# Optimization experiments

Hardware: AMD Instinct MI355X
Metric: run time of the kernel (lower is better)

The kernel has to match this reference:

```python
import jax, jax.numpy as jnp
import numpy as np

N_NODES = 50000
N_EDGES = 600000
D = 128
REL_DIM = 100
N_REL = 40
NEG_SLOPE = 0.2


def setup_inputs() -> dict:
    key = jax.random.key(0)
    ks = jax.random.split(key, 9)
    return {
        "node_features": jax.random.normal(ks[0], (N_NODES, D), jnp.float32),
        "edge_index": jax.random.randint(ks[1], (2, N_EDGES), 0, N_NODES, jnp.int64 if jax.config.jax_enable_x64 else jnp.int32),
        "edge_type": jax.random.randint(ks[2], (N_EDGES,), 0, N_REL, jnp.int32),
        "W": jax.random.normal(ks[3], (D, D), jnp.float32) * (1.0 / np.sqrt(D)),
        "W_r": jax.random.normal(ks[4], (REL_DIM, D), jnp.float32) * (1.0 / np.sqrt(REL_DIM)),
        "a": jax.random.normal(ks[5], (3 * D,), jnp.float32) * (1.0 / np.sqrt(3 * D)),
        "W_res": jax.random.normal(ks[6], (D, D), jnp.float32) * (1.0 / np.sqrt(D)),
        "b_res": jax.random.normal(ks[7], (D,), jnp.float32) * 0.01,
        "rel_emb": jax.random.normal(ks[8], (N_REL, REL_DIM), jnp.float32),
    }


def _segment_softmax(logits, seg_ids, num_segments):
    # numerically stable softmax over edges grouped by destination node
    seg_max = jax.ops.segment_max(logits, seg_ids, num_segments=num_segments)
    seg_max = jnp.where(jnp.isfinite(seg_max), seg_max, 0.0)
    e = jnp.exp(logits - seg_max[seg_ids])
    seg_sum = jax.ops.segment_sum(e, seg_ids, num_segments=num_segments)
    return e / (seg_sum[seg_ids] + 1e-16)


def reference(node_features, edge_index, edge_type, W, W_r, a, W_res, b_res, rel_emb):
    src = edge_index[0]  # x_j (source / message sender)
    dst = edge_index[1]  # x_i (target / aggregation index)

    h = node_features @ W                      # [N, D]
    h_rel = rel_emb[edge_type] @ W_r           # [E, D]
    h_src = h[src]                             # [E, D]
    h_dst = h[dst]                             # [E, D]

    # attention logit per edge: a . cat(W x_i, W x_j, W_r r_e), LeakyReLU(0.2)
    logit = h_dst @ a[:D] + h_src @ a[D:2 * D] + h_rel @ a[2 * D:]  # [E]
    logit = jax.nn.leaky_relu(logit, NEG_SLOPE)

    alpha = _segment_softmax(logit, dst, N_NODES)  # [E]

    agg = jax.ops.segment_sum(h_src * alpha[:, None], dst, num_segments=N_NODES)  # [N, D]

    out = agg + node_features @ W_res + b_res  # residual connection
    # LayerG: SELU then dropout (identity in eval mode)
    return jax.nn.selu(out)
```

## Files before the change

kernel.cpp:

```cpp
#include <hip/hip_runtime.h>
#include <hip/hip_bf16.h>

typedef __attribute__((ext_vector_type(8))) short bf16x8;
typedef __attribute__((ext_vector_type(4))) float f32x4;

#define LDS_STRIDE 528
#define CAP 64
#define TROWS 32
#define CHUNK 4096
#define BSHIFT 6
#define NBUCK_MAX 832
#define BUCKCAP 1280

__device__ __forceinline__ unsigned short f2bf(float f) {
    union { float f; unsigned int u; } v; v.f = f;
    unsigned int r = (v.u + 0x7FFF + ((v.u >> 16) & 1)) >> 16;
    return (unsigned short)r;
}
__device__ __forceinline__ float bf2f(unsigned int hbits) {
    union { unsigned int u; float f; } v; v.u = hbits << 16;
    return v.f;
}

__global__ __launch_bounds__(256) void setup_kernel(
    const float* __restrict__ W, const float* __restrict__ W_res,
    unsigned short* __restrict__ WbPack,
    const float* __restrict__ W_r, const float* __restrict__ a,
    const float* __restrict__ rel_emb, float* __restrict__ rl,
    int n_rel, int rel_dim,
    unsigned int* __restrict__ cursor, int NBUCK)
{
    __shared__ float a3[128];
    __shared__ float wa[128];
    int bid = blockIdx.x;
    int tid = threadIdx.x;

    if (bid < 16) {
        int g = bid * 256 + tid;
        int t = g >> 8;
        int s = (g >> 6) & 3;
        int lane = g & 63;
        int ncol = ((t & 7) << 4) + (lane & 15);
        int k0 = s * 32 + ((lane >> 4) << 3);
        const float* srcw = (t < 8) ? W : W_res;
        unsigned short* dstp = WbPack + ((size_t)(t * 4 + s) * 64 + lane) * 8;
        #pragma unroll
        for (int j = 0; j < 8; ++j) dstp[j] = f2bf(srcw[(size_t)(k0 + j) * 128 + ncol]);
        return;
    }
    if (bid == 16) {
        if (tid < 128) a3[tid] = a[256 + tid];
        __syncthreads();
        if (tid < rel_dim) {
            float s = 0.f;
            for (int d = 0; d < 128; ++d) s += W_r[tid * 128 + d] * a3[d];
            wa[tid] = s;
        }
        __syncthreads();
        if (tid < n_rel) {
            float s = 0.f;
            for (int k = 0; k < rel_dim; ++k) s += rel_emb[tid * rel_dim + k] * wa[k];
            rl[tid] = s;
        }
        return;
    }
    for (int i = tid; i < NBUCK; i += 256) cursor[i] = 0u;
}

__global__ __launch_bounds__(256) void gemm_scatter_kernel(
    const float* __restrict__ X, const unsigned short* __restrict__ WbPack,
    const float* __restrict__ b_res, const float* __restrict__ a,
    unsigned short* __restrict__ hb, unsigned short* __restrict__ resb,
    float* __restrict__ p, float* __restrict__ q, int M,
    const int* __restrict__ src, const int* __restrict__ dst_i, const int* __restrict__ etype,
    unsigned int* __restrict__ cursor, unsigned int* __restrict__ binned,
    int E, int NC, int NBUCK)
{
    __shared__ __align__(16) unsigned char smem[TROWS * LDS_STRIDE];
    __shared__ float pq_s[128];
    const int tid = threadIdx.x;
    const int bid = blockIdx.x;

    const bool isC = (bid < 2 * NC) && (bid & 1);
    if (isC) {
        const int k = bid >> 1;
        unsigned int* hist = (unsigned int*)smem;
        unsigned int* offs = hist + NBUCK_MAX;
        for (int i = tid; i < NBUCK; i += 256) hist[i] = 0;
        __syncthreads();
        unsigned int dcache[CHUNK / 256];
        unsigned int pk1[CHUNK / 256];
        #pragma unroll
        for (int i = 0; i < CHUNK / 256; ++i) {
            int e = k * CHUNK + i * 256 + tid;
            dcache[i] = 0xffffffffu;
            if (e < E) {
                unsigned int d = (unsigned int)__builtin_nontemporal_load(dst_i + e);
                unsigned int s = (unsigned int)__builtin_nontemporal_load(src + e);
                unsigned int t = (unsigned int)__builtin_nontemporal_load(etype + e);
                pk1[i] = (s << 16) | ((t & 63u) << 10);
                unsigned int r = atomicAdd(&hist[d >> BSHIFT], 1u);
                dcache[i] = (r << 20) | d;
            }
        }
        __syncthreads();
        for (int i = tid; i < NBUCK; i += 256) {
            unsigned int h = hist[i];
            offs[i] = h ? atomicAdd(&cursor[i], h) : 0u;
        }
        __syncthreads();
        #pragma unroll
        for (int i = 0; i < CHUNK / 256; ++i) {
            unsigned int dc = dcache[i];
            if (dc != 0xffffffffu) {
                unsigned int d = dc & 0xfffffu;
                unsigned int bk = d >> BSHIFT;
                unsigned int r = (dc >> 20) + offs[bk];
                if (r < BUCKCAP)
                    binned[(size_t)bk * BUCKCAP + r] = pk1[i] | (d & 63u);
            }
        }
        return;
    }
    const int gid = (bid < 2 * NC) ? (bid >> 1) : (bid - NC);

    const int lane = tid & 63;
    const int wave = tid >> 6;
    const int rowbase = gid * TROWS;
    const int c16 = lane & 15;
    const int kq = lane >> 4;

    if (tid < 128) pq_s[tid] = 0.f;

    bf16x8 wfrag[4][4];
    #pragma unroll
    for (int tt = 0; tt < 4; ++tt)
        #pragma unroll
        for (int s = 0; s < 4; ++s)
            wfrag[tt][s] = *(const bf16x8*)(WbPack + ((size_t)((wave * 4 + tt) * 4 + s) * 64 + lane) * 8);

    float bres[4];
    #pragma unroll
    for (int tt = 0; tt < 4; ++tt) {
        int t = wave * 4 + tt;
        bres[tt] = (t >= 8) ? b_res[(t - 8) * 16 + c16] : 0.f;
    }
    float pa[4], qa[4];
    #pragma unroll
    for (int tt = 0; tt < 4; ++tt) {
        int col = (wave * 4 + tt) * 16 + c16;
        pa[tt] = (wave < 2) ? a[col] : 0.f;
        qa[tt] = (wave < 2) ? a[128 + col] : 0.f;
    }

    #pragma unroll
    for (int j = 0; j < (TROWS * 32) / 256; ++j) {
        int ch = j * 256 + tid;
        int r = ch >> 5;
        int c = ch & 31;
        int gr = rowbase + r; if (gr >= M) gr = M - 1;
        float4 v = *(const float4*)(X + (size_t)gr * 128 + c * 4);
        unsigned int u0 = ((unsigned)f2bf(v.y) << 16) | f2bf(v.x);
        unsigned int u1 = ((unsigned)f2bf(v.w) << 16) | f2bf(v.z);
        *(uint2*)(smem + r * LDS_STRIDE + c * 8) = make_uint2(u0, u1);
    }
    __syncthreads();

    f32x4 acc[2][4];
    #pragma unroll
    for (int rt = 0; rt < 2; ++rt)
        #pragma unroll
        for (int tt = 0; tt < 4; ++tt) acc[rt][tt] = (f32x4){0.f, 0.f, 0.f, 0.f};

    #pragma unroll
    for (int s = 0; s < 4; ++s) {
        #pragma unroll
        for (int rt = 0; rt < 2; ++rt) {
            int row = rt * 16 + c16;
            bf16x8 af = *(const bf16x8*)(smem + row * LDS_STRIDE + s * 64 + kq * 16);
            #pragma unroll
            for (int tt = 0; tt < 4; ++tt)
                acc[rt][tt] = __builtin_amdgcn_mfma_f32_16x16x32_bf16(af, wfrag[tt][s], acc[rt][tt], 0, 0, 0);
        }
    }
    __syncthreads();

    if (wave < 2) {
        #pragma unroll
        for (int rt = 0; rt < 2; ++rt) {
            #pragma unroll
            for (int i = 0; i < 4; ++i) {
                float pp = 0.f, qq = 0.f;
                #pragma unroll
                for (int tt = 0; tt < 4; ++tt) {
                    pp += acc[rt][tt][i] * pa[tt];
                    qq += acc[rt][tt][i] * qa[tt];
                }
                #pragma unroll
                for (int d = 1; d < 16; d <<= 1) {
                    pp += __shfl_xor(pp, d, 64);
                    qq += __shfl_xor(qq, d, 64);
                }
                if (c16 == 0) {
                    int r = rt * 16 + kq * 4 + i;
                    atomicAdd(&pq_s[r], pp);
                    atomicAdd(&pq_s[64 + r], qq);
                }
            }
        }
    }

    #pragma unroll
    for (int rt = 0; rt < 2; ++rt) {
        #pragma unroll
        for (int tt = 0; tt < 4; ++tt) {
            int colall = (wave * 4 + tt) * 16 + c16;
            #pragma unroll
            for (int i = 0; i < 4; ++i) {
                int row = rt * 16 + kq * 4 + i;
                *(unsigned short*)(smem + row * LDS_STRIDE + colall * 2) = f2bf(acc[rt][tt][i] + bres[tt]);
            }
        }
    }
    __syncthreads();

    #pragma unroll
    for (int j = 0; j < (TROWS * 16) / 256; ++j) {
        int ch = j * 256 + tid;
        int r = ch >> 4;
        int c = ch & 15;
        int gr = rowbase + r;
        uint4 hv = *(const uint4*)(smem + r * LDS_STRIDE + c * 16);
        uint4 rv = *(const uint4*)(smem + r * LDS_STRIDE + 256 + c * 16);
        if (gr < M) {
            *(uint4*)(hb + (size_t)gr * 128 + c * 8) = hv;
            *(uint4*)(resb + (size_t)gr * 128 + c * 8) = rv;
        }
    }
    if (tid < TROWS) {
        int gr = rowbase + tid;
        if (gr < M) { p[gr] = pq_s[tid]; q[gr] = pq_s[64 + tid]; }
    }
}

__global__ __launch_bounds__(512) void agg_kernel(
    const unsigned short* __restrict__ hb, const unsigned short* __restrict__ resb,
    const float* __restrict__ p, const float* __restrict__ q, const float* __restrict__ rl,
    const unsigned int* __restrict__ binned, const unsigned int* __restrict__ cursor,
    float* __restrict__ out, int N, int n_rel)
{
    __shared__ unsigned int slots_l[64 * CAP];
    __shared__ unsigned int cnt_l[64];
    __shared__ float rls[64];
    const int tid = threadIdx.x;
    const int b = blockIdx.x;

    if (tid < n_rel) rls[tid] = rl[tid];
    if (tid < 64) cnt_l[tid] = 0;
    __syncthreads();

    const size_t off = (size_t)b * BUCKCAP;
    const unsigned int tot = min(cursor[b], (unsigned int)BUCKCAP);
    for (unsigned int i = tid; i < tot; i += 512) {
        unsigned int pk = binned[off + i];
        unsigned int dl = pk & 63u;
        unsigned int r = atomicAdd(&cnt_l[dl], 1u);
        if (r < CAP) slots_l[dl * CAP + r] = pk;
    }
    __syncthreads();

    const int lane = tid & 63;
    const int wave = tid >> 6;
    const int sub = lane & 31;
    const int shbase = lane & 32;
    const unsigned short* hsub = hb + sub * 4;

    for (int round = 0; round < 4; ++round) {
        int dl = round * 16 + wave * 2 + (lane >> 5);
        int node = b * 64 + dl;
        if (node >= N) continue;
        int nn = min((int)cnt_l[dl], CAP);

        float pnode = p[node];
        uint2 rv = *(const uint2*)(resb + (size_t)node * 128 + sub * 4);
        float a0 = 0.f, a1 = 0.f, a2 = 0.f, a3 = 0.f;
        float ssum = 0.f;

        for (int c = 0; c < nn; c += 32) {
            int m = min(32, nn - c);
            float se = 0.f;
            int sv = 0;
            if (sub < m) {
                unsigned int pk = slots_l[dl * CAP + c + sub];
                sv = (int)(pk >> 16);
                int t = (int)((pk >> 10) & 63u);
                float l = pnode + q[sv] + rls[t];
                l = (l > 0.f) ? l : 0.2f * l;
                se = __expf(l);
            }
            ssum += se;

            int j = 0;
            for (; j + 7 < m; j += 8) {
                float w[8]; int r[8]; uint2 v[8];
                #pragma unroll
                for (int u = 0; u < 8; ++u) { w[u] = __shfl(se, shbase + j + u); r[u] = __shfl(sv, shbase + j + u); }
                #pragma unroll
                for (int u = 0; u < 8; ++u) v[u] = *(const uint2*)(hsub + (size_t)r[u] * 128);
                #pragma unroll
                for (int u = 0; u < 8; ++u) {
                    a0 += w[u] * bf2f(v[u].x & 0xffff);
                    a1 += w[u] * bf2f(v[u].x >> 16);
                    a2 += w[u] * bf2f(v[u].y & 0xffff);
                    a3 += w[u] * bf2f(v[u].y >> 16);
                }
            }
            for (; j + 3 < m; j += 4) {
                float w[4]; int r[4]; uint2 v[4];
                #pragma unroll
                for (int u = 0; u < 4; ++u) { w[u] = __shfl(se, shbase + j + u); r[u] = __shfl(sv, shbase + j + u); }
                #pragma unroll
                for (int u = 0; u < 4; ++u) v[u] = *(const uint2*)(hsub + (size_t)r[u] * 128);
                #pragma unroll
                for (int u = 0; u < 4; ++u) {
                    a0 += w[u] * bf2f(v[u].x & 0xffff);
                    a1 += w[u] * bf2f(v[u].x >> 16);
                    a2 += w[u] * bf2f(v[u].y & 0xffff);
                    a3 += w[u] * bf2f(v[u].y >> 16);
                }
            }
            for (; j < m; ++j) {
                float w = __shfl(se, shbase + j);
                int r = __shfl(sv, shbase + j);
                uint2 v = *(const uint2*)(hsub + (size_t)r * 128);
                a0 += w * bf2f(v.x & 0xffff);
                a1 += w * bf2f(v.x >> 16);
                a2 += w * bf2f(v.y & 0xffff);
                a3 += w * bf2f(v.y >> 16);
            }
        }

        #pragma unroll
        for (int d = 1; d < 32; d <<= 1) ssum += __shfl_xor(ssum, d, 64);
        float inv = 1.0f / (ssum + 1e-16f);
        a0 *= inv; a1 *= inv; a2 *= inv; a3 *= inv;

        float o0 = a0 + bf2f(rv.x & 0xffff), o1 = a1 + bf2f(rv.x >> 16);
        float o2 = a2 + bf2f(rv.y & 0xffff), o3 = a3 + bf2f(rv.y >> 16);
        const float SC = 1.0507009873554805f, AL = 1.6732632423543772f;
        o0 = (o0 > 0.f) ? SC * o0 : SC * AL * (__expf(o0) - 1.f);
        o1 = (o1 > 0.f) ? SC * o1 : SC * AL * (__expf(o1) - 1.f);
        o2 = (o2 > 0.f) ? SC * o2 : SC * AL * (__expf(o2) - 1.f);
        o3 = (o3 > 0.f) ? SC * o3 : SC * AL * (__expf(o3) - 1.f);
        f32x4 ov = (f32x4){o0, o1, o2, o3};
        __builtin_nontemporal_store(ov, (f32x4*)(out + (size_t)node * 128 + sub * 4));
    }
}

extern "C" void kernel_launch(void* const* d_in, const int* in_sizes, int n_in,
                              void* d_out, int out_size, void* d_ws, size_t ws_size,
                              hipStream_t stream)
{
    const float* X      = (const float*)d_in[0];
    const int*   ei     = (const int*)d_in[1];
    const int*   etype  = (const int*)d_in[2];
    const float* W      = (const float*)d_in[3];
    const float* W_r    = (const float*)d_in[4];
    const float* a      = (const float*)d_in[5];
    const float* W_res  = (const float*)d_in[6];
    const float* b_res  = (const float*)d_in[7];
    const float* rel_emb= (const float*)d_in[8];

    const int N = in_sizes[0] / 128;
    const int E = in_sizes[2];
    const int n_rel = in_sizes[8] / 100;
    const int* src = ei;
    const int* dst = ei + E;

    char* w = (char*)d_ws;
    auto alloc = [&](size_t bytes) -> void* {
        void* ptr = (void*)w;
        w += (bytes + 255) & ~(size_t)255;
        return ptr;
    };
    const int NC    = (E + CHUNK - 1) / CHUNK;
    const int NBUCK = (N + 63) >> BSHIFT;

    unsigned short* WbPack = (unsigned short*)alloc((size_t)16 * 4 * 64 * 8 * 2);
    unsigned short* hb     = (unsigned short*)alloc((size_t)N * 128 * 2);
    unsigned short* resb   = (unsigned short*)alloc((size_t)N * 128 * 2);
    float* p       = (float*)alloc((size_t)N * 4);
    float* q       = (float*)alloc((size_t)N * 4);
    float* rl      = (float*)alloc(64 * 4);
    unsigned int* cursor = (unsigned int*)alloc((size_t)NBUCK * 4);
    unsigned int* binned = (unsigned int*)alloc((size_t)NBUCK * BUCKCAP * 4);
    float* out     = (float*)d_out;

    const int gemm_blocks = (N + TROWS - 1) / TROWS;
    const int agg_blocks  = NBUCK;

    setup_kernel<<<18, 256, 0, stream>>>(W, W_res, WbPack, W_r, a, rel_emb, rl,
                                         n_rel, 100, cursor, NBUCK);
    gemm_scatter_kernel<<<gemm_blocks + NC, 256, 0, stream>>>(
        X, WbPack, b_res, a, hb, resb, p, q, N,
        src, dst, etype, cursor, binned, E, NC, NBUCK);
    agg_kernel<<<agg_blocks, 512, 0, stream>>>(hb, resb, p, q, rl, binned, cursor,
                                               out, N, n_rel);
}
```

Baseline: 147.5 us.

## Replace global bucket cursors with per-chunk fixed cells in edge binning

```diff
diff --git a/kernel.cpp b/kernel.cpp
--- a/kernel.cpp
+++ b/kernel.cpp
@@ -10,7 +10,7 @@
 #define CHUNK 4096
 #define BSHIFT 6
 #define NBUCK_MAX 832
-#define BUCKCAP 1280
+#define CELLCAP 32
 
 __device__ __forceinline__ unsigned short f2bf(float f) {
     union { float f; unsigned int u; } v; v.f = f;
@@ -27,8 +27,7 @@
     unsigned short* __restrict__ WbPack,
     const float* __restrict__ W_r, const float* __restrict__ a,
     const float* __restrict__ rel_emb, float* __restrict__ rl,
-    int n_rel, int rel_dim,
-    unsigned int* __restrict__ cursor, int NBUCK)
+    int n_rel, int rel_dim)
 {
     __shared__ float a3[128];
     __shared__ float wa[128];
@@ -48,23 +47,19 @@
         for (int j = 0; j < 8; ++j) dstp[j] = f2bf(srcw[(size_t)(k0 + j) * 128 + ncol]);
         return;
     }
-    if (bid == 16) {
-        if (tid < 128) a3[tid] = a[256 + tid];
-        __syncthreads();
-        if (tid < rel_dim) {
-            float s = 0.f;
-            for (int d = 0; d < 128; ++d) s += W_r[tid * 128 + d] * a3[d];
-            wa[tid] = s;
-        }
-        __syncthreads();
-        if (tid < n_rel) {
-            float s = 0.f;
-            for (int k = 0; k < rel_dim; ++k) s += rel_emb[tid * rel_dim + k] * wa[k];
-            rl[tid] = s;
-        }
-        return;
-    }
-    for (int i = tid; i < NBUCK; i += 256) cursor[i] = 0u;
+    if (tid < 128) a3[tid] = a[256 + tid];
+    __syncthreads();
+    if (tid < rel_dim) {
+        float s = 0.f;
+        for (int d = 0; d < 128; ++d) s += W_r[tid * 128 + d] * a3[d];
+        wa[tid] = s;
+    }
+    __syncthreads();
+    if (tid < n_rel) {
+        float s = 0.f;
+        for (int k = 0; k < rel_dim; ++k) s += rel_emb[tid * rel_dim + k] * wa[k];
+        rl[tid] = s;
+    }
 }
 
 __global__ __launch_bounds__(256) void gemm_scatter_kernel(
@@ -73,7 +68,7 @@
     unsigned short* __restrict__ hb, unsigned short* __restrict__ resb,
     float* __restrict__ p, float* __restrict__ q, int M,
     const int* __restrict__ src, const int* __restrict__ dst_i, const int* __restrict__ etype,
-    unsigned int* __restrict__ cursor, unsigned int* __restrict__ binned,
+    unsigned char* __restrict__ cnt, unsigned int* __restrict__ binned,
     int E, int NC, int NBUCK)
 {
     __shared__ __align__(16) unsigned char smem[TROWS * LDS_STRIDE];
@@ -85,7 +80,6 @@
     if (isC) {
         const int k = bid >> 1;
         unsigned int* hist = (unsigned int*)smem;
-        unsigned int* offs = hist + NBUCK_MAX;
         for (int i = tid; i < NBUCK; i += 256) hist[i] = 0;
         __syncthreads();
         unsigned int dcache[CHUNK / 256];
@@ -104,20 +98,17 @@
             }
         }
         __syncthreads();
-        for (int i = tid; i < NBUCK; i += 256) {
-            unsigned int h = hist[i];
-            offs[i] = h ? atomicAdd(&cursor[i], h) : 0u;
-        }
-        __syncthreads();
+        for (int i = tid; i < NBUCK; i += 256)
+            cnt[(size_t)i * NC + k] = (unsigned char)min(hist[i], 255u);
         #pragma unroll
         for (int i = 0; i < CHUNK / 256; ++i) {
             unsigned int dc = dcache[i];
             if (dc != 0xffffffffu) {
                 unsigned int d = dc & 0xfffffu;
                 unsigned int bk = d >> BSHIFT;
-                unsigned int r = (dc >> 20) + offs[bk];
-                if (r < BUCKCAP)
-                    binned[(size_t)bk * BUCKCAP + r] = pk1[i] | (d & 63u);
+                unsigned int r = dc >> 20;
+                if (r < CELLCAP)
+                    binned[((size_t)bk * NC + k) * CELLCAP + r] = pk1[i] | (d & 63u);
             }
         }
         return;
@@ -246,26 +237,30 @@
 __global__ __launch_bounds__(512) void agg_kernel(
     const unsigned short* __restrict__ hb, const unsigned short* __restrict__ resb,
     const float* __restrict__ p, const float* __restrict__ q, const float* __restrict__ rl,
-    const unsigned int* __restrict__ binned, const unsigned int* __restrict__ cursor,
-    float* __restrict__ out, int N, int n_rel)
+    const unsigned int* __restrict__ binned, const unsigned char* __restrict__ cnt,
+    float* __restrict__ out, int N, int n_rel, int NC)
 {
     __shared__ unsigned int slots_l[64 * CAP];
     __shared__ unsigned int cnt_l[64];
+    __shared__ unsigned char cntl[160];
     __shared__ float rls[64];
     const int tid = threadIdx.x;
     const int b = blockIdx.x;
 
     if (tid < n_rel) rls[tid] = rl[tid];
     if (tid < 64) cnt_l[tid] = 0;
-    __syncthreads();
-
-    const size_t off = (size_t)b * BUCKCAP;
-    const unsigned int tot = min(cursor[b], (unsigned int)BUCKCAP);
-    for (unsigned int i = tid; i < tot; i += 512) {
-        unsigned int pk = binned[off + i];
-        unsigned int dl = pk & 63u;
-        unsigned int r = atomicAdd(&cnt_l[dl], 1u);
-        if (r < CAP) slots_l[dl * CAP + r] = pk;
+    if (tid < NC) cntl[tid] = cnt[(size_t)b * NC + tid];
+    __syncthreads();
+
+    if (tid < NC) {
+        int n = min((int)cntl[tid], CELLCAP);
+        const unsigned int* cell = binned + ((size_t)b * NC + tid) * CELLCAP;
+        for (int j = 0; j < n; ++j) {
+            unsigned int pk = cell[j];
+            unsigned int dl = pk & 63u;
+            unsigned int r = atomicAdd(&cnt_l[dl], 1u);
+            if (r < CAP) slots_l[dl * CAP + r] = pk;
+        }
     }
     __syncthreads();
 
@@ -392,18 +387,18 @@
     float* p       = (float*)alloc((size_t)N * 4);
     float* q       = (float*)alloc((size_t)N * 4);
     float* rl      = (float*)alloc(64 * 4);
-    unsigned int* cursor = (unsigned int*)alloc((size_t)NBUCK * 4);
-    unsigned int* binned = (unsigned int*)alloc((size_t)NBUCK * BUCKCAP * 4);
+    unsigned char* cnt   = (unsigned char*)alloc((size_t)NBUCK * NC);
+    unsigned int* binned = (unsigned int*)alloc((size_t)NBUCK * NC * CELLCAP * 4);
     float* out     = (float*)d_out;
 
     const int gemm_blocks = (N + TROWS - 1) / TROWS;
     const int agg_blocks  = NBUCK;
 
-    setup_kernel<<<18, 256, 0, stream>>>(W, W_res, WbPack, W_r, a, rel_emb, rl,
-                                         n_rel, 100, cursor, NBUCK);
+    setup_kernel<<<17, 256, 0, stream>>>(W, W_res, WbPack, W_r, a, rel_emb, rl,
+                                         n_rel, 100);
     gemm_scatter_kernel<<<gemm_blocks + NC, 256, 0, stream>>>(
         X, WbPack, b_res, a, hb, resb, p, q, N,
-        src, dst, etype, cursor, binned, E, NC, NBUCK);
-    agg_kernel<<<agg_blocks, 512, 0, stream>>>(hb, resb, p, q, rl, binned, cursor,
-                                               out, N, n_rel);
-}
+        src, dst, etype, cnt, binned, E, NC, NBUCK);
+    agg_kernel<<<agg_blocks, 512, 0, stream>>>(hb, resb, p, q, rl, binned, cnt,
+                                               out, N, n_rel, NC);
+}
```

Measured after the change: 153.7 us. +4.3%, slower.

## Fuse setup, GEMM/scatter and aggregation into one cooperative persistent kernel

Applied to the files above, without the earlier changes.

```diff
diff --git a/kernel.cpp b/kernel.cpp
--- a/kernel.cpp
+++ b/kernel.cpp
@@ -1,5 +1,8 @@
 #include <hip/hip_runtime.h>
 #include <hip/hip_bf16.h>
+#include <hip/hip_cooperative_groups.h>
+
+namespace cg = cooperative_groups;
 
 typedef __attribute__((ext_vector_type(8))) short bf16x8;
 typedef __attribute__((ext_vector_type(4))) float f32x4;
@@ -22,338 +25,332 @@
     return v.f;
 }
 
-__global__ __launch_bounds__(256) void setup_kernel(
+__global__ __launch_bounds__(256) void fused_all(
+    const float* __restrict__ X,
     const float* __restrict__ W, const float* __restrict__ W_res,
+    const float* __restrict__ W_r, const float* __restrict__ av,
+    const float* __restrict__ b_res, const float* __restrict__ rel_emb,
+    const int* __restrict__ srcI, const int* __restrict__ dstI, const int* __restrict__ etypeI,
     unsigned short* __restrict__ WbPack,
-    const float* __restrict__ W_r, const float* __restrict__ a,
-    const float* __restrict__ rel_emb, float* __restrict__ rl,
-    int n_rel, int rel_dim,
-    unsigned int* __restrict__ cursor, int NBUCK)
+    unsigned short* __restrict__ hb, unsigned short* __restrict__ resb,
+    float* __restrict__ p, float* __restrict__ q, float* __restrict__ rl,
+    unsigned int* __restrict__ cursor, unsigned int* __restrict__ binned,
+    float* __restrict__ out,
+    int Nn, int E, int n_rel, int rel_dim, int NC, int NBUCK, int GT)
 {
-    __shared__ float a3[128];
-    __shared__ float wa[128];
-    int bid = blockIdx.x;
-    int tid = threadIdx.x;
-
-    if (bid < 16) {
-        int g = bid * 256 + tid;
-        int t = g >> 8;
-        int s = (g >> 6) & 3;
-        int lane = g & 63;
-        int ncol = ((t & 7) << 4) + (lane & 15);
-        int k0 = s * 32 + ((lane >> 4) << 3);
-        const float* srcw = (t < 8) ? W : W_res;
-        unsigned short* dstp = WbPack + ((size_t)(t * 4 + s) * 64 + lane) * 8;
-        #pragma unroll
-        for (int j = 0; j < 8; ++j) dstp[j] = f2bf(srcw[(size_t)(k0 + j) * 128 + ncol]);
-        return;
-    }
-    if (bid == 16) {
-        if (tid < 128) a3[tid] = a[256 + tid];
-        __syncthreads();
-        if (tid < rel_dim) {
-            float s = 0.f;
-            for (int d = 0; d < 128; ++d) s += W_r[tid * 128 + d] * a3[d];
-            wa[tid] = s;
-        }
-        __syncthreads();
-        if (tid < n_rel) {
-            float s = 0.f;
-            for (int k = 0; k < rel_dim; ++k) s += rel_emb[tid * rel_dim + k] * wa[k];
-            rl[tid] = s;
-        }
-        return;
-    }
-    for (int i = tid; i < NBUCK; i += 256) cursor[i] = 0u;
-}
-
-__global__ __launch_bounds__(256) void gemm_scatter_kernel(
-    const float* __restrict__ X, const unsigned short* __restrict__ WbPack,
-    const float* __restrict__ b_res, const float* __restrict__ a,
-    unsigned short* __restrict__ hb, unsigned short* __restrict__ resb,
-    float* __restrict__ p, float* __restrict__ q, int M,
-    const int* __restrict__ src, const int* __restrict__ dst_i, const int* __restrict__ etype,
-    unsigned int* __restrict__ cursor, unsigned int* __restrict__ binned,
-    int E, int NC, int NBUCK)
-{
+    cg::grid_group grid = cg::this_grid();
     __shared__ __align__(16) unsigned char smem[TROWS * LDS_STRIDE];
     __shared__ float pq_s[128];
-    const int tid = threadIdx.x;
-    const int bid = blockIdx.x;
-
-    const bool isC = (bid < 2 * NC) && (bid & 1);
-    if (isC) {
-        const int k = bid >> 1;
-        unsigned int* hist = (unsigned int*)smem;
-        unsigned int* offs = hist + NBUCK_MAX;
-        for (int i = tid; i < NBUCK; i += 256) hist[i] = 0;
-        __syncthreads();
-        unsigned int dcache[CHUNK / 256];
-        unsigned int pk1[CHUNK / 256];
-        #pragma unroll
-        for (int i = 0; i < CHUNK / 256; ++i) {
-            int e = k * CHUNK + i * 256 + tid;
-            dcache[i] = 0xffffffffu;
-            if (e < E) {
-                unsigned int d = (unsigned int)__builtin_nontemporal_load(dst_i + e);
-                unsigned int s = (unsigned int)__builtin_nontemporal_load(src + e);
-                unsigned int t = (unsigned int)__builtin_nontemporal_load(etype + e);
-                pk1[i] = (s << 16) | ((t & 63u) << 10);
-                unsigned int r = atomicAdd(&hist[d >> BSHIFT], 1u);
-                dcache[i] = (r << 20) | d;
-            }
-        }
-        __syncthreads();
-        for (int i = tid; i < NBUCK; i += 256) {
-            unsigned int h = hist[i];
-            offs[i] = h ? atomicAdd(&cursor[i], h) : 0u;
-        }
-        __syncthreads();
-        #pragma unroll
-        for (int i = 0; i < CHUNK / 256; ++i) {
-            unsigned int dc = dcache[i];
-            if (dc != 0xffffffffu) {
-                unsigned int d = dc & 0xfffffu;
-                unsigned int bk = d >> BSHIFT;
-                unsigned int r = (dc >> 20) + offs[bk];
-                if (r < BUCKCAP)
-                    binned[(size_t)bk * BUCKCAP + r] = pk1[i] | (d & 63u);
-            }
-        }
-        return;
-    }
-    const int gid = (bid < 2 * NC) ? (bid >> 1) : (bid - NC);
-
-    const int lane = tid & 63;
-    const int wave = tid >> 6;
-    const int rowbase = gid * TROWS;
-    const int c16 = lane & 15;
-    const int kq = lane >> 4;
-
-    if (tid < 128) pq_s[tid] = 0.f;
-
-    bf16x8 wfrag[4][4];
-    #pragma unroll
-    for (int tt = 0; tt < 4; ++tt)
-        #pragma unroll
-        for (int s = 0; s < 4; ++s)
-            wfrag[tt][s] = *(const bf16x8*)(WbPack + ((size_t)((wave * 4 + tt) * 4 + s) * 64 + lane) * 8);
-
-    float bres[4];
-    #pragma unroll
-    for (int tt = 0; tt < 4; ++tt) {
-        int t = wave * 4 + tt;
-        bres[tt] = (t >= 8) ? b_res[(t - 8) * 16 + c16] : 0.f;
-    }
-    float pa[4], qa[4];
-    #pragma unroll
-    for (int tt = 0; tt < 4; ++tt) {
-        int col = (wave * 4 + tt) * 16 + c16;
-        pa[tt] = (wave < 2) ? a[col] : 0.f;
-        qa[tt] = (wave < 2) ? a[128 + col] : 0.f;
-    }
-
-    #pragma unroll
-    for (int j = 0; j < (TROWS * 32) / 256; ++j) {
-        int ch = j * 256 + tid;
-        int r = ch >> 5;
-        int c = ch & 31;
-        int gr = rowbase + r; if (gr >= M) gr = M - 1;
-        float4 v = *(const float4*)(X + (size_t)gr * 128 + c * 4);
-        unsigned int u0 = ((unsigned)f2bf(v.y) << 16) | f2bf(v.x);
-        unsigned int u1 = ((unsigned)f2bf(v.w) << 16) | f2bf(v.z);
-        *(uint2*)(smem + r * LDS_STRIDE + c * 8) = make_uint2(u0, u1);
-    }
-    __syncthreads();
-
-    f32x4 acc[2][4];
-    #pragma unroll
-    for (int rt = 0; rt < 2; ++rt)
-        #pragma unroll
-        for (int tt = 0; tt < 4; ++tt) acc[rt][tt] = (f32x4){0.f, 0.f, 0.f, 0.f};
-
-    #pragma unroll
-    for (int s = 0; s < 4; ++s) {
-        #pragma unroll
-        for (int rt = 0; rt < 2; ++rt) {
-            int row = rt * 16 + c16;
-            bf16x8 af = *(const bf16x8*)(smem + row * LDS_STRIDE + s * 64 + kq * 16);
-            #pragma unroll
-            for (int tt = 0; tt < 4; ++tt)
-                acc[rt][tt] = __builtin_amdgcn_mfma_f32_16x16x32_bf16(af, wfrag[tt][s], acc[rt][tt], 0, 0, 0);
-        }
-    }
-    __syncthreads();
-
-    if (wave < 2) {
-        #pragma unroll
-        for (int rt = 0; rt < 2; ++rt) {
-            #pragma unroll
-            for (int i = 0; i < 4; ++i) {
-                float pp = 0.f, qq = 0.f;
-                #pragma unroll
-                for (int tt = 0; tt < 4; ++tt) {
-                    pp += acc[rt][tt][i] * pa[tt];
-                    qq += acc[rt][tt][i] * qa[tt];
-                }
-                #pragma unroll
-                for (int d = 1; d < 16; d <<= 1) {
-                    pp += __shfl_xor(pp, d, 64);
-                    qq += __shfl_xor(qq, d, 64);
-                }
-                if (c16 == 0) {
-                    int r = rt * 16 + kq * 4 + i;
-                    atomicAdd(&pq_s[r], pp);
-                    atomicAdd(&pq_s[64 + r], qq);
-                }
-            }
-        }
-    }
-
-    #pragma unroll
-    for (int rt = 0; rt < 2; ++rt) {
-        #pragma unroll
-        for (int tt = 0; tt < 4; ++tt) {
-            int colall = (wave * 4 + tt) * 16 + c16;
-            #pragma unroll
-            for (int i = 0; i < 4; ++i) {
-                int row = rt * 16 + kq * 4 + i;
-                *(unsigned short*)(smem + row * LDS_STRIDE + colall * 2) = f2bf(acc[rt][tt][i] + bres[tt]);
-            }
-        }
-    }
-    __syncthreads();
-
-    #pragma unroll
-    for (int j = 0; j < (TROWS * 16) / 256; ++j) {
-        int ch = j * 256 + tid;
-        int r = ch >> 4;
-        int c = ch & 15;
-        int gr = rowbase + r;
-        uint4 hv = *(const uint4*)(smem + r * LDS_STRIDE + c * 16);
-        uint4 rv = *(const uint4*)(smem + r * LDS_STRIDE + 256 + c * 16);
-        if (gr < M) {
-            *(uint4*)(hb + (size_t)gr * 128 + c * 8) = hv;
-            *(uint4*)(resb + (size_t)gr * 128 + c * 8) = rv;
-        }
-    }
-    if (tid < TROWS) {
-        int gr = rowbase + tid;
-        if (gr < M) { p[gr] = pq_s[tid]; q[gr] = pq_s[64 + tid]; }
-    }
-}
-
-__global__ __launch_bounds__(512) void agg_kernel(
-    const unsigned short* __restrict__ hb, const unsigned short* __restrict__ resb,
-    const float* __restrict__ p, const float* __restrict__ q, const float* __restrict__ rl,
-    const unsigned int* __restrict__ binned, const unsigned int* __restrict__ cursor,
-    float* __restrict__ out, int N, int n_rel)
-{
-    __shared__ unsigned int slots_l[64 * CAP];
     __shared__ unsigned int cnt_l[64];
     __shared__ float rls[64];
     const int tid = threadIdx.x;
-    const int b = blockIdx.x;
+    const int nblk = gridDim.x;
+
+    {
+        const int bid = blockIdx.x;
+        if (bid < 16) {
+            int g = bid * 256 + tid;
+            int t = g >> 8;
+            int s = (g >> 6) & 3;
+            int lane = g & 63;
+            int ncol = ((t & 7) << 4) + (lane & 15);
+            int k0 = s * 32 + ((lane >> 4) << 3);
+            const float* srcw = (t < 8) ? W : W_res;
+            unsigned short* dstp = WbPack + ((size_t)(t * 4 + s) * 64 + lane) * 8;
+            #pragma unroll
+            for (int j = 0; j < 8; ++j) dstp[j] = f2bf(srcw[(size_t)(k0 + j) * 128 + ncol]);
+        } else if (bid == 16) {
+            float* a3 = (float*)smem;
+            float* wa = a3 + 128;
+            if (tid < 128) a3[tid] = av[256 + tid];
+            __syncthreads();
+            if (tid < rel_dim) {
+                float s = 0.f;
+                for (int d = 0; d < 128; ++d) s += W_r[tid * 128 + d] * a3[d];
+                wa[tid] = s;
+            }
+            __syncthreads();
+            if (tid < n_rel) {
+                float s = 0.f;
+                for (int k = 0; k < rel_dim; ++k) s += rel_emb[tid * rel_dim + k] * wa[k];
+                rl[tid] = s;
+            }
+        } else if (bid == 17) {
+            for (int i = tid; i < NBUCK; i += 256) cursor[i] = 0u;
+        }
+    }
+    __threadfence();
+    grid.sync();
+    __threadfence();
+
+    for (int item = blockIdx.x; item < NC + GT; item += nblk) {
+        __syncthreads();
+        if (item < NC) {
+            const int k = item;
+            unsigned int* hist = (unsigned int*)smem;
+            unsigned int* offs = hist + NBUCK_MAX;
+            for (int i = tid; i < NBUCK; i += 256) hist[i] = 0;
+            __syncthreads();
+            unsigned int dcache[CHUNK / 256];
+            unsigned int pk1[CHUNK / 256];
+            #pragma unroll
+            for (int i = 0; i < CHUNK / 256; ++i) {
+                int e = k * CHUNK + i * 256 + tid;
+                dcache[i] = 0xffffffffu;
+                if (e < E) {
+                    unsigned int d = (unsigned int)__builtin_nontemporal_load(dstI + e);
+                    unsigned int s = (unsigned int)__builtin_nontemporal_load(srcI + e);
+                    unsigned int t = (unsigned int)__builtin_nontemporal_load(etypeI + e);
+                    pk1[i] = (s << 16) | ((t & 63u) << 10);
+                    unsigned int r = atomicAdd(&hist[d >> BSHIFT], 1u);
+                    dcache[i] = (r << 20) | d;
+                }
+            }
+            __syncthreads();
+            for (int i = tid; i < NBUCK; i += 256) {
+                unsigned int h = hist[i];
+                offs[i] = h ? atomicAdd(&cursor[i], h) : 0u;
+            }
+            __syncthreads();
+            #pragma unroll
+            for (int i = 0; i < CHUNK / 256; ++i) {
+                unsigned int dc = dcache[i];
+                if (dc != 0xffffffffu) {
+                    unsigned int d = dc & 0xfffffu;
+                    unsigned int bk = d >> BSHIFT;
+                    unsigned int r = (dc >> 20) + offs[bk];
+                    if (r < BUCKCAP)
+                        binned[(size_t)bk * BUCKCAP + r] = pk1[i] | (d & 63u);
+                }
+            }
+        } else {
+            const int gid = item - NC;
+            const int lane = tid & 63;
+            const int wave = tid >> 6;
+            const int rowbase = gid * TROWS;
+            const int c16 = lane & 15;
+            const int kq = lane >> 4;
+
+            if (tid < 128) pq_s[tid] = 0.f;
+
+            bf16x8 wfrag[4][4];
+            #pragma unroll
+            for (int tt = 0; tt < 4; ++tt)
+                #pragma unroll
+                for (int s = 0; s < 4; ++s)
+                    wfrag[tt][s] = *(const bf16x8*)(WbPack + ((size_t)((wave * 4 + tt) * 4 + s) * 64 + lane) * 8);
+
+            float bres[4];
+            #pragma unroll
+            for (int tt = 0; tt < 4; ++tt) {
+                int t = wave * 4 + tt;
+                bres[tt] = (t >= 8) ? b_res[(t - 8) * 16 + c16] : 0.f;
+            }
+            float pa[4], qa[4];
+            #pragma unroll
+            for (int tt = 0; tt < 4; ++tt) {
+                int col = (wave * 4 + tt) * 16 + c16;
+                pa[tt] = (wave < 2) ? av[col] : 0.f;
+                qa[tt] = (wave < 2) ? av[128 + col] : 0.f;
+            }
+
+            #pragma unroll
+            for (int j = 0; j < (TROWS * 32) / 256; ++j) {
+                int ch = j * 256 + tid;
+                int r = ch >> 5;
+                int c = ch & 31;
+                int gr = rowbase + r; if (gr >= Nn) gr = Nn - 1;
+                float4 v = *(const float4*)(X + (size_t)gr * 128 + c * 4);
+                unsigned int u0 = ((unsigned)f2bf(v.y) << 16) | f2bf(v.x);
+                unsigned int u1 = ((unsigned)f2bf(v.w) << 16) | f2bf(v.z);
+                *(uint2*)(smem + r * LDS_STRIDE + c * 8) = make_uint2(u0, u1);
+            }
+            __syncthreads();
+
+            f32x4 acc[2][4];
+            #pragma unroll
+            for (int rt = 0; rt < 2; ++rt)
+                #pragma unroll
+                for (int tt = 0; tt < 4; ++tt) acc[rt][tt] = (f32x4){0.f, 0.f, 0.f, 0.f};
+
+            #pragma unroll
+            for (int s = 0; s < 4; ++s) {
+                #pragma unroll
+                for (int rt = 0; rt < 2; ++rt) {
+                    int row = rt * 16 + c16;
+                    bf16x8 af = *(const bf16x8*)(smem + row * LDS_STRIDE + s * 64 + kq * 16);
+                    #pragma unroll
+                    for (int tt = 0; tt < 4; ++tt)
+                        acc[rt][tt] = __builtin_amdgcn_mfma_f32_16x16x32_bf16(af, wfrag[tt][s], acc[rt][tt], 0, 0, 0);
+                }
+            }
+            __syncthreads();
+
+            if (wave < 2) {
+                #pragma unroll
+                for (int rt = 0; rt < 2; ++rt) {
+                    #pragma unroll
+                    for (int i = 0; i < 4; ++i) {
+                        float pp = 0.f, qq = 0.f;
+                        #pragma unroll
+                        for (int tt = 0; tt < 4; ++tt) {
+                            pp += acc[rt][tt][i] * pa[tt];
+                            qq += acc[rt][tt][i] * qa[tt];
+                        }
+                        #pragma unroll
+                        for (int d = 1; d < 16; d <<= 1) {
+                            pp += __shfl_xor(pp, d, 64);
+                            qq += __shfl_xor(qq, d, 64);
+                        }
+                        if (c16 == 0) {
+                            int r = rt * 16 + kq * 4 + i;
+                            atomicAdd(&pq_s[r], pp);
+                            atomicAdd(&pq_s[64 + r], qq);
+                        }
+                    }
+                }
+            }
+
+            #pragma unroll
+            for (int rt = 0; rt < 2; ++rt) {
+                #pragma unroll
+                for (int tt = 0; tt < 4; ++tt) {
+                    int colall = (wave * 4 + tt) * 16 + c16;
+                    #pragma unroll
+                    for (int i = 0; i < 4; ++i) {
+                        int row = rt * 16 + kq * 4 + i;
+                        *(unsigned short*)(smem + row * LDS_STRIDE + colall * 2) = f2bf(acc[rt][tt][i] + bres[tt]);
+                    }
+                }
+            }
+            __syncthreads();
+
+            #pragma unroll
+            for (int j = 0; j < (TROWS * 16) / 256; ++j) {
+                int ch = j * 256 + tid;
+                int r = ch >> 4;
+                int c = ch & 15;
+                int gr = rowbase + r;
+                uint4 hv = *(const uint4*)(smem + r * LDS_STRIDE + c * 16);
+                uint4 rv = *(const uint4*)(smem + r * LDS_STRIDE + 256 + c * 16);
+                if (gr < Nn) {
+                    *(uint4*)(hb + (size_t)gr * 128 + c * 8) = hv;
+                    *(uint4*)(resb + (size_t)gr * 128 + c * 8) = rv;
+                }
+            }
+            if (tid < TROWS) {
+                int gr = rowbase + tid;
+                if (gr < Nn) { p[gr] = pq_s[tid]; q[gr] = pq_s[64 + tid]; }
+            }
+        }
+    }
+    __threadfence();
+    grid.sync();
+    __threadfence();
 
     if (tid < n_rel) rls[tid] = rl[tid];
-    if (tid < 64) cnt_l[tid] = 0;
-    __syncthreads();
-
-    const size_t off = (size_t)b * BUCKCAP;
-    const unsigned int tot = min(cursor[b], (unsigned int)BUCKCAP);
-    for (unsigned int i = tid; i < tot; i += 512) {
-        unsigned int pk = binned[off + i];
-        unsigned int dl = pk & 63u;
-        unsigned int r = atomicAdd(&cnt_l[dl], 1u);
-        if (r < CAP) slots_l[dl * CAP + r] = pk;
-    }
-    __syncthreads();
-
+    unsigned int* slots_l = (unsigned int*)smem;
     const int lane = tid & 63;
     const int wave = tid >> 6;
     const int sub = lane & 31;
     const int shbase = lane & 32;
     const unsigned short* hsub = hb + sub * 4;
 
-    for (int round = 0; round < 4; ++round) {
-        int dl = round * 16 + wave * 2 + (lane >> 5);
-        int node = b * 64 + dl;
-        if (node >= N) continue;
-        int nn = min((int)cnt_l[dl], CAP);
-
-        float pnode = p[node];
-        uint2 rv = *(const uint2*)(resb + (size_t)node * 128 + sub * 4);
-        float a0 = 0.f, a1 = 0.f, a2 = 0.f, a3 = 0.f;
-        float ssum = 0.f;
-
-        for (int c = 0; c < nn; c += 32) {
-            int m = min(32, nn - c);
-            float se = 0.f;
-            int sv = 0;
-            if (sub < m) {
-                unsigned int pk = slots_l[dl * CAP + c + sub];
-                sv = (int)(pk >> 16);
-                int t = (int)((pk >> 10) & 63u);
-                float l = pnode + q[sv] + rls[t];
-                l = (l > 0.f) ? l : 0.2f * l;
-                se = __expf(l);
-            }
-            ssum += se;
-
-            int j = 0;
-            for (; j + 7 < m; j += 8) {
-                float w[8]; int r[8]; uint2 v[8];
-                #pragma unroll
-                for (int u = 0; u < 8; ++u) { w[u] = __shfl(se, shbase + j + u); r[u] = __shfl(sv, shbase + j + u); }
-                #pragma unroll
-                for (int u = 0; u < 8; ++u) v[u] = *(const uint2*)(hsub + (size_t)r[u] * 128);
-                #pragma unroll
-                for (int u = 0; u < 8; ++u) {
-                    a0 += w[u] * bf2f(v[u].x & 0xffff);
-                    a1 += w[u] * bf2f(v[u].x >> 16);
-                    a2 += w[u] * bf2f(v[u].y & 0xffff);
-                    a3 += w[u] * bf2f(v[u].y >> 16);
-                }
-            }
-            for (; j + 3 < m; j += 4) {
-                float w[4]; int r[4]; uint2 v[4];
-                #pragma unroll
-                for (int u = 0; u < 4; ++u) { w[u] = __shfl(se, shbase + j + u); r[u] = __shfl(sv, shbase + j + u); }
-                #pragma unroll
-                for (int u = 0; u < 4; ++u) v[u] = *(const uint2*)(hsub + (size_t)r[u] * 128);
-                #pragma unroll
-                for (int u = 0; u < 4; ++u) {
-                    a0 += w[u] * bf2f(v[u].x & 0xffff);
-                    a1 += w[u] * bf2f(v[u].x >> 16);
-                    a2 += w[u] * bf2f(v[u].y & 0xffff);
-                    a3 += w[u] * bf2f(v[u].y >> 16);
-                }
-            }
-            for (; j < m; ++j) {
-                float w = __shfl(se, shbase + j);
-                int r = __shfl(sv, shbase + j);
-                uint2 v = *(const uint2*)(hsub + (size_t)r * 128);
-                a0 += w * bf2f(v.x & 0xffff);
-                a1 += w * bf2f(v.x >> 16);
-                a2 += w * bf2f(v.y & 0xffff);
-                a3 += w * bf2f(v.y >> 16);
-            }
+    for (int b = blockIdx.x; b < NBUCK; b += nblk) {
+        if (tid < 64) cnt_l[tid] = 0;
+        __syncthreads();
+
+        const size_t off = (size_t)b * BUCKCAP;
+        const unsigned int tot = min(cursor[b], (unsigned int)BUCKCAP);
+        for (unsigned int i = tid; i < tot; i += 256) {
+            unsigned int pk = binned[off + i];
+            unsigned int dl = pk & 63u;
+            unsigned int r = atomicAdd(&cnt_l[dl], 1u);
+            if (r < CAP) slots_l[dl * CAP + r] = pk;
         }
-
-        #pragma unroll
-        for (int d = 1; d < 32; d <<= 1) ssum += __shfl_xor(ssum, d, 64);
-        float inv = 1.0f / (ssum + 1e-16f);
-        a0 *= inv; a1 *= inv; a2 *= inv; a3 *= inv;
-
-        float o0 = a0 + bf2f(rv.x & 0xffff), o1 = a1 + bf2f(rv.x >> 16);
-        float o2 = a2 + bf2f(rv.y & 0xffff), o3 = a3 + bf2f(rv.y >> 16);
-        const float SC = 1.0507009873554805f, AL = 1.6732632423543772f;
-        o0 = (o0 > 0.f) ? SC * o0 : SC * AL * (__expf(o0) - 1.f);
-        o1 = (o1 > 0.f) ? SC * o1 : SC * AL * (__expf(o1) - 1.f);
-        o2 = (o2 > 0.f) ? SC * o2 : SC * AL * (__expf(o2) - 1.f);
-        o3 = (o3 > 0.f) ? SC * o3 : SC * AL * (__expf(o3) - 1.f);
-        f32x4 ov = (f32x4){o0, o1, o2, o3};
-        __builtin_nontemporal_store(ov, (f32x4*)(out + (size_t)node * 128 + sub * 4));
+        __syncthreads();
+
+        for (int round = 0; round < 8; ++round) {
+            int dl = round * 8 + wave * 2 + (lane >> 5);
+            int node = b * 64 + dl;
+            if (node < Nn) {
+                int nn = min((int)cnt_l[dl], CAP);
+                float pnode = p[node];
+                uint2 rv = *(const uint2*)(resb + (size_t)node * 128 + sub * 4);
+                float a0 = 0.f, a1 = 0.f, a2 = 0.f, a3 = 0.f;
+                float ssum = 0.f;
+
+                for (int c = 0; c < nn; c += 32) {
+                    int m = min(32, nn - c);
+                    float se = 0.f;
+                    int sv = 0;
+                    if (sub < m) {
+                        unsigned int pk = slots_l[dl * CAP + c + sub];
+                        sv = (int)(pk >> 16);
+                        int t = (int)((pk >> 10) & 63u);
+                        float l = pnode + q[sv] + rls[t];
+                        l = (l > 0.f) ? l : 0.2f * l;
+                        se = __expf(l);
+                    }
+                    ssum += se;
+
+                    int j = 0;
+                    for (; j + 7 < m; j += 8) {
+                        float w[8]; int r[8]; uint2 v[8];
+                        #pragma unroll
+                        for (int u = 0; u < 8; ++u) { w[u] = __shfl(se, shbase + j + u); r[u] = __shfl(sv, shbase + j + u); }
+                        #pragma unroll
+                        for (int u = 0; u < 8; ++u) v[u] = *(const uint2*)(hsub + (size_t)r[u] * 128);
+                        #pragma unroll
+                        for (int u = 0; u < 8; ++u) {
+                            a0 += w[u] * bf2f(v[u].x & 0xffff);
+                            a1 += w[u] * bf2f(v[u].x >> 16);
+                            a2 += w[u] * bf2f(v[u].y & 0xffff);
+                            a3 += w[u] * bf2f(v[u].y >> 16);
+                        }
+                    }
+                    for (; j + 3 < m; j += 4) {
+                        float w[4]; int r[4]; uint2 v[4];
+                        #pragma unroll
+                        for (int u = 0; u < 4; ++u) { w[u] = __shfl(se, shbase + j + u); r[u] = __shfl(sv, shbase + j + u); }
+                        #pragma unroll
+                        for (int u = 0; u < 4; ++u) v[u] = *(const uint2*)(hsub + (size_t)r[u] * 128);
+                        #pragma unroll
+                        for (int u = 0; u < 4; ++u) {
+                            a0 += w[u] * bf2f(v[u].x & 0xffff);
+                            a1 += w[u] * bf2f(v[u].x >> 16);
+                            a2 += w[u] * bf2f(v[u].y & 0xffff);
+                            a3 += w[u] * bf2f(v[u].y >> 16);
+                        }
+                    }
+                    for (; j < m; ++j) {
+                        float w = __shfl(se, shbase + j);
+                        int r = __shfl(sv, shbase + j);
+                        uint2 v = *(const uint2*)(hsub + (size_t)r * 128);
+                        a0 += w * bf2f(v.x & 0xffff);
+                        a1 += w * bf2f(v.x >> 16);
+                        a2 += w * bf2f(v.y & 0xffff);
+                        a3 += w * bf2f(v.y >> 16);
+                    }
+                }
+
+                #pragma unroll
+                for (int d = 1; d < 32; d <<= 1) ssum += __shfl_xor(ssum, d, 64);
+                float inv = 1.0f / (ssum + 1e-16f);
+                a0 *= inv; a1 *= inv; a2 *= inv; a3 *= inv;
+
+                float o0 = a0 + bf2f(rv.x & 0xffff), o1 = a1 + bf2f(rv.x >> 16);
+                float o2 = a2 + bf2f(rv.y & 0xffff), o3 = a3 + bf2f(rv.y >> 16);
+                const float SC = 1.0507009873554805f, AL = 1.6732632423543772f;
+                o0 = (o0 > 0.f) ? SC * o0 : SC * AL * (__expf(o0) - 1.f);
+                o1 = (o1 > 0.f) ? SC * o1 : SC * AL * (__expf(o1) - 1.f);
+                o2 = (o2 > 0.f) ? SC * o2 : SC * AL * (__expf(o2) - 1.f);
+                o3 = (o3 > 0.f) ? SC * o3 : SC * AL * (__expf(o3) - 1.f);
+                f32x4 ov = (f32x4){o0, o1, o2, o3};
+                __builtin_nontemporal_store(ov, (f32x4*)(out + (size_t)node * 128 + sub * 4));
+            }
+        }
+        __syncthreads();
     }
 }
 
@@ -373,7 +370,7 @@
 
     const int N = in_sizes[0] / 128;
     const int E = in_sizes[2];
-    const int n_rel = in_sizes[8] / 100;
+    int n_rel = in_sizes[8] / 100;
     const int* src = ei;
     const int* dst = ei + E;
 
@@ -383,8 +380,9 @@
         w += (bytes + 255) & ~(size_t)255;
         return ptr;
     };
-    const int NC    = (E + CHUNK - 1) / CHUNK;
-    const int NBUCK = (N + 63) >> BSHIFT;
+    int NC    = (E + CHUNK - 1) / CHUNK;
+    int NBUCK = (N + 63) >> BSHIFT;
+    int GT    = (N + TROWS - 1) / TROWS;
 
     unsigned short* WbPack = (unsigned short*)alloc((size_t)16 * 4 * 64 * 8 * 2);
     unsigned short* hb     = (unsigned short*)alloc((size_t)N * 128 * 2);
@@ -396,14 +394,26 @@
     unsigned int* binned = (unsigned int*)alloc((size_t)NBUCK * BUCKCAP * 4);
     float* out     = (float*)d_out;
 
-    const int gemm_blocks = (N + TROWS - 1) / TROWS;
-    const int agg_blocks  = NBUCK;
-
-    setup_kernel<<<18, 256, 0, stream>>>(W, W_res, WbPack, W_r, a, rel_emb, rl,
-                                         n_rel, 100, cursor, NBUCK);
-    gemm_scatter_kernel<<<gemm_blocks + NC, 256, 0, stream>>>(
-        X, WbPack, b_res, a, hb, resb, p, q, N,
-        src, dst, etype, cursor, binned, E, NC, NBUCK);
-    agg_kernel<<<agg_blocks, 512, 0, stream>>>(hb, resb, p, q, rl, binned, cursor,
-                                               out, N, n_rel);
+    int maxb = 0;
+    if (hipOccupancyMaxActiveBlocksPerMultiprocessor(&maxb, (const void*)fused_all, 256, 0)
+            != hipSuccess || maxb < 1)
+        maxb = 4;
+    long G = (long)maxb * 256;
+    const long need = (long)NC + GT;
+    if (G > need) G = need;
+    if (G < 64) G = 64;
+
+    int Nn = N, Ee = E, rdim = 100;
+    void* kargs[] = {
+        (void*)&X, (void*)&W, (void*)&W_res, (void*)&W_r, (void*)&a,
+        (void*)&b_res, (void*)&rel_emb,
+        (void*)&src, (void*)&dst, (void*)&etype,
+        (void*)&WbPack, (void*)&hb, (void*)&resb,
+        (void*)&p, (void*)&q, (void*)&rl,
+        (void*)&cursor, (void*)&binned, (void*)&out,
+        (void*)&Nn, (void*)&Ee, (void*)&n_rel, (void*)&rdim,
+        (void*)&NC, (void*)&NBUCK, (void*)&GT
+    };
+    hipLaunchCooperativeKernel((void*)fused_all, dim3((unsigned)G), dim3(256),
+                               kargs, 0, stream);
 }
```

Result: slower. 388.2 us (+163.3%).
